# Kernel tuning notes

Measured on AMD Instinct MI355X. Metric: run time of the kernel, lower is better.

## Reference

```python
import math
import jax, jax.numpy as jnp
import numpy as np

NUM_BUCKETS = 32
MAX_DISTANCE = 128
N_HEADS = 16
D_KV = 64


def _relative_position_bucket(relative_position, num_buckets=NUM_BUCKETS, max_distance=MAX_DISTANCE):
    # bidirectional (encoder) version, faithful to T5Attention._relative_position_bucket
    nb = num_buckets // 2
    rel_buckets = (relative_position > 0).astype(jnp.int32) * nb
    rp = jnp.abs(relative_position)
    max_exact = nb // 2
    is_small = rp < max_exact
    # log-spaced buckets for large distances; clamp arg of log to >=1 to avoid -inf
    rp_large = max_exact + (
        jnp.log(jnp.maximum(rp, 1).astype(jnp.float32) / max_exact)
        / math.log(max_distance / max_exact)
        * (nb - max_exact)
    ).astype(jnp.int32)
    rp_large = jnp.minimum(rp_large, nb - 1)
    return rel_buckets + jnp.where(is_small, rp, rp_large)


def setup_inputs() -> dict:
    key = jax.random.key(0)
    ks = jax.random.split(key, 6)
    B, S, D = 2, 2048, 1024
    scale = 0.02
    return {
        "hidden_states": jax.random.normal(ks[0], (B, S, D), dtype=jnp.float32),
        "Wq": jax.random.normal(ks[1], (D, N_HEADS * D_KV), dtype=jnp.float32) * scale,
        "Wk": jax.random.normal(ks[2], (D, N_HEADS * D_KV), dtype=jnp.float32) * scale,
        "Wv": jax.random.normal(ks[3], (D, N_HEADS * D_KV), dtype=jnp.float32) * scale,
        "Wo": jax.random.normal(ks[4], (N_HEADS * D_KV, D), dtype=jnp.float32) * scale,
        "rel_bias": jax.random.normal(ks[5], (NUM_BUCKETS, N_HEADS), dtype=jnp.float32),
    }


def reference(hidden_states, Wq, Wk, Wv, Wo, rel_bias):
    B, S, D = hidden_states.shape
    H, dk = N_HEADS, D_KV
    q = (hidden_states @ Wq).reshape(B, S, H, dk)
    k = (hidden_states @ Wk).reshape(B, S, H, dk)
    v = (hidden_states @ Wv).reshape(B, S, H, dk)

    pos = jnp.arange(S)
    relative_position = pos[None, :] - pos[:, None]          # [S_q, S_k]
    buckets = _relative_position_bucket(relative_position)    # [S_q, S_k]
    bias = rel_bias[buckets].transpose(2, 0, 1)               # [H, S_q, S_k]

    # T5 attention: NO 1/sqrt(d) scaling
    scores = jnp.einsum('bqhd,bkhd->bhqk', q, k) + bias[None]
    attn = jax.nn.softmax(scores, axis=-1)
    ctx = jnp.einsum('bhqk,bkhd->bqhd', attn, v).reshape(B, S, H * dk)
    return ctx @ Wo
```

## Files before the change

kernel.cpp:

```cpp
#include <hip/hip_runtime.h>
#include <stdint.h>

#define S_LEN 2048
#define NH 16
#define NB_DELTA (2*S_LEN-1)
#define PST 72

typedef __attribute__((ext_vector_type(8))) __bf16 bf16x8;
typedef __attribute__((ext_vector_type(4))) float f32x4;

__device__ __forceinline__ unsigned short f2bf(float f){
    union { float f; unsigned int u; } v; v.f = f;
    unsigned int u = v.u;
    return (unsigned short)((u + 0x7FFFu + ((u >> 16) & 1u)) >> 16);
}
__device__ __forceinline__ unsigned short f2bf_fast(float f){
    union { float f; unsigned int u; } v; v.f = f;
    return (unsigned short)((v.u + 0x8000u) >> 16);
}
__device__ __forceinline__ float bf2f(unsigned short u){
    union { unsigned int u; float f; } v; v.u = ((unsigned int)u) << 16;
    return v.f;
}

__device__ __forceinline__ void gload16(const void* g, void* l){
    __builtin_amdgcn_global_load_lds(
        (const __attribute__((address_space(1))) void*)(uintptr_t)g,
        (__attribute__((address_space(3))) void*)(uintptr_t)l, 16, 0, 0);
}

__global__ __launch_bounds__(256) void prep_kernel(
    const float* __restrict__ hs, unsigned short* __restrict__ hsb,
    const float* __restrict__ W0, const float* __restrict__ W1,
    const float* __restrict__ W2, const float* __restrict__ W3,
    unsigned short* __restrict__ D0, unsigned short* __restrict__ D1,
    unsigned short* __restrict__ D2, unsigned short* __restrict__ D3,
    const float* __restrict__ rel_bias, float* __restrict__ biasT){
    if (blockIdx.z == 4) {
        int bi = blockIdx.y * 32 + blockIdx.x;
        for (int it = 0; it < 4; it++) {
            int i = bi * 4096 + it * 1024 + threadIdx.x * 4;
            float4 f = *(const float4*)(hs + i);
            ushort4 o;
            o.x = f2bf(f.x); o.y = f2bf(f.y); o.z = f2bf(f.z); o.w = f2bf(f.w);
            *(ushort4*)(hsb + i) = o;
        }
        if (bi < 16) {
            int t = bi * 256 + threadIdx.x;
            if (t < NB_DELTA) {
                int delta = t - (S_LEN - 1);
                int bucket = (delta > 0) ? 16 : 0;
                int a = delta < 0 ? -delta : delta;
                int b;
                if (a < 8) b = a;
                else {
                    int bl = 33 - __builtin_clz(a * a);
                    b = bl < 15 ? bl : 15;
                }
                bucket += b;
                for (int h = 0; h < NH; h++)
                    biasT[h * NB_DELTA + t] = rel_bias[bucket * NH + h];
            }
        }
        return;
    }
    const float* src; unsigned short* dst;
    switch (blockIdx.z) {
        case 0: src = W0; dst = D0; break;
        case 1: src = W1; dst = D1; break;
        case 2: src = W2; dst = D2; break;
        default: src = W3; dst = D3; break;
    }
    __shared__ float tile[32][33];
    int bx = blockIdx.x, by = blockIdx.y;
    int tx = threadIdx.x & 31, ty = threadIdx.x >> 5;
    for (int i = 0; i < 4; i++)
        tile[ty + 8*i][tx] = src[(size_t)(by*32 + ty + 8*i) * 1024 + bx*32 + tx];
    __syncthreads();
    for (int i = 0; i < 4; i++)
        dst[(size_t)(bx*32 + ty + 8*i) * 1024 + by*32 + tx] = f2bf(tile[tx][ty + 8*i]);
}

template<int MODE, int BM>
__global__ __launch_bounds__(256) void gemm_bt_kernel(const unsigned short* __restrict__ A,
                                                      const unsigned short* __restrict__ BT,
                                                      float* __restrict__ C0,
                                                      unsigned short* __restrict__ C1,
                                                      int Kdim, int ldc){
    constexpr int IT = BM / 32;
    __shared__ __align__(16) unsigned short As[BM * 64];
    __shared__ __align__(16) unsigned short Bs[128 * 64];
    const int t = threadIdx.x;
    const int wave = t >> 6, lane = t & 63;
    const int quad = lane >> 4, l16 = lane & 15;
    const int wm = (wave >> 1) * (BM / 2), wn = (wave & 1) * 64;
    const size_t row0 = (size_t)blockIdx.y * BM, col0 = (size_t)blockIdx.x * 128;

    const int srow8 = lane >> 3;
    const int gg = (lane & 7) ^ srow8;
    const unsigned short* gA = A  + (row0 + wave * 8 + srow8) * (size_t)Kdim + gg * 8;
    const unsigned short* gB = BT + (col0 + wave * 8 + srow8) * (size_t)Kdim + gg * 8;

    f32x4 acc[IT][4] = {};

    for (int kt = 0; kt < Kdim; kt += 64) {
        for (int p = 0; p < BM / 32; p++)
            gload16(gA + (size_t)(p * 32) * Kdim + kt, &As[(p * 32 + wave * 8) * 64]);
        for (int p = 0; p < 4; p++)
            gload16(gB + (size_t)(p * 32) * Kdim + kt, &Bs[(p * 32 + wave * 8) * 64]);
        __syncthreads();
        bf16x8 a[2][IT], b[2][4];
        for (int ks = 0; ks < 2; ks++) {
            for (int i = 0; i < IT; i++)
                a[ks][i] = *(const bf16x8*)(&As[(wm + i*16 + l16) * 64 + (((ks*4 + quad) ^ (l16 & 7)) * 8)]);
            for (int j = 0; j < 4; j++)
                b[ks][j] = *(const bf16x8*)(&Bs[(wn + j*16 + l16) * 64 + (((ks*4 + quad) ^ (l16 & 7)) * 8)]);
        }
        for (int ks = 0; ks < 2; ks++)
            for (int i = 0; i < IT; i++)
                for (int j = 0; j < 4; j++)
                    acc[i][j] = __builtin_amdgcn_mfma_f32_16x16x32_bf16(a[ks][i], b[ks][j], acc[i][j], 0, 0, 0);
        __syncthreads();
    }
    for (int i = 0; i < IT; i++)
        for (int j = 0; j < 4; j++) {
            size_t r0 = row0 + wm + i*16 + quad*4;
            size_t c  = col0 + wn + j*16 + l16;
            if (MODE == 0) {
                for (int r = 0; r < 4; r++)
                    C0[(r0 + r) * ldc + c] = acc[i][j][r];
            } else {
                for (int r = 0; r < 4; r++)
                    C1[(r0 + r) * ldc + c] = f2bf(acc[i][j][r]);
            }
        }
}

__global__ __launch_bounds__(256) void vtrans_kernel(const unsigned short* __restrict__ qkv,
                                                     unsigned short* __restrict__ vt){
    __shared__ unsigned short tile[64][72];
    const int v0 = blockIdx.x * 64, s0 = blockIdx.y * 64, b = blockIdx.z;
    const int tx = threadIdx.x & 7, ty = threadIdx.x >> 3;
    for (int i = 0; i < 2; i++)
        *(int4*)&tile[ty + 32*i][tx * 8] =
            *(const int4*)(qkv + (size_t)(b * 2048 + s0 + ty + 32*i) * 3072 + 2048 + v0 + tx * 8);
    __syncthreads();
    for (int i = 0; i < 2; i++) {
        int v = ty + 32*i;
        int sl = tx * 8;
        ushort4 o0, o1;
        o0.x = tile[sl+0][v]; o0.y = tile[sl+1][v]; o0.z = tile[sl+2][v]; o0.w = tile[sl+3][v];
        o1.x = tile[sl+4][v]; o1.y = tile[sl+5][v]; o1.z = tile[sl+6][v]; o1.w = tile[sl+7][v];
        unsigned short* dst = vt + (size_t)(b * 1024 + v0 + v) * 2048 + s0 + sl;
        *(ushort4*)dst = o0; *(ushort4*)(dst + 4) = o1;
    }
}

__global__ __launch_bounds__(256, 4) void flash7_kernel(
    const unsigned short* __restrict__ qkv,
    const unsigned short* __restrict__ vt,
    const float* __restrict__ biasT,
    unsigned short* __restrict__ ctxpb,
    float* __restrict__ rsbuf)
{
    const int qt = blockIdx.x, h = blockIdx.y;
    const int b = blockIdx.z >> 1, ck = blockIdx.z & 1;
    const int kt0 = ck << 10;
    const int t = threadIdx.x;
    const int w = t >> 6, lane = t & 63, quad = lane >> 4, l16 = lane & 15;
    const int q0 = qt * 128;

    __shared__ __align__(16) unsigned short Ks[64 * 64];
    __shared__ __align__(16) unsigned short Vs[64 * 64];
    __shared__ __align__(16) unsigned short Pb[128 * PST];
    __shared__ float bias_s[192];

    for (int s = 0; s < 4; s++) {
        int g = t + s * 256;
        int r = g >> 3, c = (g & 7) * 8;
        *(int4*)&Pb[r * PST + c] =
            *(const int4*)(qkv + (size_t)(b * S_LEN + q0 + r) * 3072 + h * 64 + c);
    }
    __syncthreads();
    bf16x8 qb[2][2];
    for (int nt = 0; nt < 2; nt++)
        for (int ks = 0; ks < 2; ks++)
            qb[ks][nt] = *(const bf16x8*)&Pb[(w * 32 + nt * 16 + l16) * PST + ks * 32 + quad * 8];

    float rsum[2] = {0.f, 0.f};
    f32x4 ctx[4][2] = {};

    const float* biasRow = biasT + h * NB_DELTA + 2047;

    const int srow8 = lane >> 3;
    const int gg = (lane & 7) ^ srow8;
    const int swz = ((l16 & 7) * 8);

    for (int kt = kt0; kt < kt0 + 1024; kt += 64) {
        __syncthreads();
        {
            const unsigned short* kb = qkv + (size_t)(b * S_LEN + kt + w * 8 + srow8) * 3072 + 1024 + h * 64 + gg * 8;
            const unsigned short* vb = vt + (size_t)(b * 1024 + h * 64 + w * 8 + srow8) * 2048 + kt + gg * 8;
            gload16(kb,                         &Ks[(w * 8) * 64]);
            gload16(kb + (size_t)32 * 3072,     &Ks[(32 + w * 8) * 64]);
            gload16(vb,                         &Vs[(w * 8) * 64]);
            gload16(vb + (size_t)32 * 2048,     &Vs[(32 + w * 8) * 64]);
            if (t < 192) bias_s[t] = biasRow[kt - q0 - 127 + t] - 16.0f;
        }
        __syncthreads();

        f32x4 st[4][2] = {};
        for (int ks = 0; ks < 2; ks++)
            for (int nb = 0; nb < 4; nb++) {
                bf16x8 ka = *(const bf16x8*)&Ks[(nb * 16 + l16) * 64 + (((ks * 4 + quad) * 8) ^ swz)];
                st[nb][0] = __builtin_amdgcn_mfma_f32_16x16x32_bf16(ka, qb[ks][0], st[nb][0], 0, 0, 0);
                st[nb][1] = __builtin_amdgcn_mfma_f32_16x16x32_bf16(ka, qb[ks][1], st[nb][1], 0, 0, 0);
            }
        for (int nt = 0; nt < 2; nt++) {
            const int ib = quad * 4 + 127 - w * 32 - nt * 16 - l16;
            float rs = 0.f;
            for (int nb = 0; nb < 4; nb++) {
                float e0 = __expf(st[nb][nt][0] + bias_s[ib + nb * 16 + 0]);
                float e1 = __expf(st[nb][nt][1] + bias_s[ib + nb * 16 + 1]);
                float e2 = __expf(st[nb][nt][2] + bias_s[ib + nb * 16 + 2]);
                float e3 = __expf(st[nb][nt][3] + bias_s[ib + nb * 16 + 3]);
                rs += (e0 + e1) + (e2 + e3);
                ushort4 pk;
                pk.x = f2bf_fast(e0); pk.y = f2bf_fast(e1);
                pk.z = f2bf_fast(e2); pk.w = f2bf_fast(e3);
                *(ushort4*)&Pb[(w * 32 + nt * 16 + l16) * PST + nb * 16 + quad * 4] = pk;
            }
            rsum[nt] += rs;
        }
        for (int ks = 0; ks < 2; ks++) {
            bf16x8 pb0 = *(const bf16x8*)&Pb[(w * 32 + l16) * PST + ks * 32 + quad * 8];
            bf16x8 pb1 = *(const bf16x8*)&Pb[(w * 32 + 16 + l16) * PST + ks * 32 + quad * 8];
            for (int nd = 0; nd < 4; nd++) {
                bf16x8 va = *(const bf16x8*)&Vs[(nd * 16 + l16) * 64 + (((ks * 4 + quad) * 8) ^ swz)];
                ctx[nd][0] = __builtin_amdgcn_mfma_f32_16x16x32_bf16(va, pb0, ctx[nd][0], 0, 0, 0);
                ctx[nd][1] = __builtin_amdgcn_mfma_f32_16x16x32_bf16(va, pb1, ctx[nd][1], 0, 0, 0);
            }
        }
    }
    unsigned short* cp = ctxpb + (size_t)ck * 4096 * 1024;
    for (int nt = 0; nt < 2; nt++) {
        float rs = rsum[nt];
        rs += __shfl_xor(rs, 16, 64);
        rs += __shfl_xor(rs, 32, 64);
        int row = b * S_LEN + q0 + w * 32 + nt * 16 + l16;
        if (quad == 0) rsbuf[((size_t)ck * 4096 + row) * 16 + h] = rs;
        for (int nd = 0; nd < 4; nd++) {
            ushort4 pk;
            pk.x = f2bf(ctx[nd][nt][0]); pk.y = f2bf(ctx[nd][nt][1]);
            pk.z = f2bf(ctx[nd][nt][2]); pk.w = f2bf(ctx[nd][nt][3]);
            *(ushort4*)&cp[(size_t)row * 1024 + h * 64 + nd * 16 + quad * 4] = pk;
        }
    }
}

__global__ __launch_bounds__(256) void combine_kernel(const unsigned short* __restrict__ ctxpb,
                                                      const float* __restrict__ rsbuf,
                                                      unsigned short* __restrict__ ctxb){
    int e = blockIdx.x * 256 + threadIdx.x;
    int row = e >> 8;
    int c4 = (e & 255) * 4;
    int h = c4 >> 6;
    float l = rsbuf[(size_t)row * 16 + h] + rsbuf[((size_t)4096 + row) * 16 + h];
    ushort4 a  = *(const ushort4*)&ctxpb[(size_t)row * 1024 + c4];
    ushort4 b2 = *(const ushort4*)&ctxpb[(size_t)4096 * 1024 + (size_t)row * 1024 + c4];
    float inv = 1.f / l;
    ushort4 o;
    o.x = f2bf((bf2f(a.x) + bf2f(b2.x)) * inv);
    o.y = f2bf((bf2f(a.y) + bf2f(b2.y)) * inv);
    o.z = f2bf((bf2f(a.z) + bf2f(b2.z)) * inv);
    o.w = f2bf((bf2f(a.w) + bf2f(b2.w)) * inv);
    *(ushort4*)&ctxb[(size_t)row * 1024 + c4] = o;
}

extern "C" void kernel_launch(void* const* d_in, const int* in_sizes, int n_in,
                              void* d_out, int out_size, void* d_ws, size_t ws_size,
                              hipStream_t stream) {
    const float* hs       = (const float*)d_in[0];
    const float* Wq       = (const float*)d_in[1];
    const float* Wk       = (const float*)d_in[2];
    const float* Wv       = (const float*)d_in[3];
    const float* Wo       = (const float*)d_in[4];
    const float* rel_bias = (const float*)d_in[5];
    float* out = (float*)d_out;

    char* ws = (char*)d_ws;
    float* biasT          = (float*)ws;           ws += 262144;
    unsigned short* hsb   = (unsigned short*)ws;  ws += 8388608;
    unsigned short* WT    = (unsigned short*)ws;  ws += 6291456;
    unsigned short* WoT   = (unsigned short*)ws;  ws += 2097152;
    unsigned short* qkvb  = (unsigned short*)ws;  ws += 25165824;
    unsigned short* Vtg   = (unsigned short*)ws;  ws += 8388608;
    unsigned short* ctxb  = (unsigned short*)ws;  ws += 8388608;
    unsigned short* ctxpb = (unsigned short*)ws;  ws += 16777216;
    float* rsbuf          = (float*)ws;

    prep_kernel<<<dim3(32, 32, 5), 256, 0, stream>>>(
        hs, hsb, Wq, Wk, Wv, Wo,
        WT, WT + 1024 * 1024, WT + 2 * 1024 * 1024, WoT, rel_bias, biasT);

    gemm_bt_kernel<1, 128><<<dim3(24, 32), 256, 0, stream>>>(hsb, WT, nullptr, qkvb, 1024, 3072);
    vtrans_kernel<<<dim3(16, 32, 2), 256, 0, stream>>>(qkvb, Vtg);
    flash7_kernel<<<dim3(S_LEN / 128, NH, 4), 256, 0, stream>>>(qkvb, Vtg, biasT, ctxpb, rsbuf);
    combine_kernel<<<4096, 256, 0, stream>>>(ctxpb, rsbuf, ctxb);
    gemm_bt_kernel<0, 64><<<dim3(8, 64), 256, 0, stream>>>(ctxb, WoT, out, nullptr, 1024, 1024);
}
```

Baseline: 207.6 us.

## Split flash warps over query and key halves, use exp2 with constant far-bias

Each warp in the attention kernel now covers 64 query rows and half of each 64-key tile (a 2x2 split instead of 4x1). This doubles how often each loaded K/V fragment is reused, and the two key-half partial contexts are reduced through shared memory at the end. Q is pre-scaled by log2(e) in the QKV GEMM epilogue so the softmax can use a native exp2. For key tiles far from the diagonal, the bias is the saturated bucket constant, so its load and the per-element lookup are skipped. Packed bf16 conversions replace the manual ones. The costs are higher register pressure (launch bound lowered to 3 blocks) and an extra shared-memory reduction.

```diff
diff --git a/kernel.cpp b/kernel.cpp
--- a/kernel.cpp
+++ b/kernel.cpp
@@ -1,10 +1,12 @@
 #include <hip/hip_runtime.h>
+#include <hip/hip_bf16.h>
 #include <stdint.h>
 
 #define S_LEN 2048
 #define NH 16
 #define NB_DELTA (2*S_LEN-1)
 #define PST 72
+#define LOG2E 1.4426950408889634f
 
 typedef __attribute__((ext_vector_type(8))) __bf16 bf16x8;
 typedef __attribute__((ext_vector_type(4))) float f32x4;
@@ -14,14 +16,21 @@
     unsigned int u = v.u;
     return (unsigned short)((u + 0x7FFFu + ((u >> 16) & 1u)) >> 16);
 }
-__device__ __forceinline__ unsigned short f2bf_fast(float f){
-    union { float f; unsigned int u; } v; v.f = f;
-    return (unsigned short)((v.u + 0x8000u) >> 16);
-}
 __device__ __forceinline__ float bf2f(unsigned short u){
     union { unsigned int u; float f; } v; v.u = ((unsigned int)u) << 16;
     return v.f;
 }
+__device__ __forceinline__ unsigned int pkbf(float a, float b){
+    __hip_bfloat162 h = __float22bfloat162_rn(float2{a, b});
+    unsigned int u;
+    __builtin_memcpy(&u, &h, 4);
+    return u;
+}
+#if __has_builtin(__builtin_amdgcn_exp2f)
+__device__ __forceinline__ float fexp2(float x){ return __builtin_amdgcn_exp2f(x); }
+#else
+__device__ __forceinline__ float fexp2(float x){ return __expf(x * 0.69314718056f); }
+#endif
 
 __device__ __forceinline__ void gload16(const void* g, void* l){
     __builtin_amdgcn_global_load_lds(
@@ -130,8 +139,9 @@
                 for (int r = 0; r < 4; r++)
                     C0[(r0 + r) * ldc + c] = acc[i][j][r];
             } else {
+                float qs = (c < 1024) ? LOG2E : 1.0f;
                 for (int r = 0; r < 4; r++)
-                    C1[(r0 + r) * ldc + c] = f2bf(acc[i][j][r]);
+                    C1[(r0 + r) * ldc + c] = f2bf(acc[i][j][r] * qs);
             }
         }
 }
@@ -156,10 +166,11 @@
     }
 }
 
-__global__ __launch_bounds__(256, 4) void flash7_kernel(
+__global__ __launch_bounds__(256, 3) void flash8_kernel(
     const unsigned short* __restrict__ qkv,
     const unsigned short* __restrict__ vt,
     const float* __restrict__ biasT,
+    const float* __restrict__ rel_bias,
     unsigned short* __restrict__ ctxpb,
     float* __restrict__ rsbuf)
 {
@@ -168,12 +179,17 @@
     const int kt0 = ck << 10;
     const int t = threadIdx.x;
     const int w = t >> 6, lane = t & 63, quad = lane >> 4, l16 = lane & 15;
+    const int qh = w & 1, jh = w >> 1;
     const int q0 = qt * 128;
 
-    __shared__ __align__(16) unsigned short Ks[64 * 64];
-    __shared__ __align__(16) unsigned short Vs[64 * 64];
-    __shared__ __align__(16) unsigned short Pb[128 * PST];
-    __shared__ float bias_s[192];
+    __shared__ __align__(16) unsigned short SMEM[18272];
+    unsigned short* Ks = SMEM;
+    unsigned short* Vs = SMEM + 4096;
+    unsigned short* Pb = SMEM + 8192;
+    float* bias_s = (float*)(SMEM + 17408);
+
+    const float b15 = (rel_bias[15 * NH + h] - 16.f) * LOG2E;
+    const float b31 = (rel_bias[31 * NH + h] - 16.f) * LOG2E;
 
     for (int s = 0; s < 4; s++) {
         int g = t + s * 256;
@@ -182,13 +198,13 @@
             *(const int4*)(qkv + (size_t)(b * S_LEN + q0 + r) * 3072 + h * 64 + c);
     }
     __syncthreads();
-    bf16x8 qb[2][2];
-    for (int nt = 0; nt < 2; nt++)
+    bf16x8 qb[2][4];
+    for (int nt = 0; nt < 4; nt++)
         for (int ks = 0; ks < 2; ks++)
-            qb[ks][nt] = *(const bf16x8*)&Pb[(w * 32 + nt * 16 + l16) * PST + ks * 32 + quad * 8];
-
-    float rsum[2] = {0.f, 0.f};
-    f32x4 ctx[4][2] = {};
+            qb[ks][nt] = *(const bf16x8*)&Pb[(qh * 64 + nt * 16 + l16) * PST + ks * 32 + quad * 8];
+
+    float rsum[4] = {0.f, 0.f, 0.f, 0.f};
+    f32x4 ctx[4][4] = {};
 
     const float* biasRow = biasT + h * NB_DELTA + 2047;
 
@@ -197,63 +213,94 @@
     const int swz = ((l16 & 7) * 8);
 
     for (int kt = kt0; kt < kt0 + 1024; kt += 64) {
+        const int off = kt - q0;
+        const bool cst = (off >= 255) || (off <= -191);
         __syncthreads();
         {
             const unsigned short* kb = qkv + (size_t)(b * S_LEN + kt + w * 8 + srow8) * 3072 + 1024 + h * 64 + gg * 8;
             const unsigned short* vb = vt + (size_t)(b * 1024 + h * 64 + w * 8 + srow8) * 2048 + kt + gg * 8;
-            gload16(kb,                         &Ks[(w * 8) * 64]);
-            gload16(kb + (size_t)32 * 3072,     &Ks[(32 + w * 8) * 64]);
-            gload16(vb,                         &Vs[(w * 8) * 64]);
-            gload16(vb + (size_t)32 * 2048,     &Vs[(32 + w * 8) * 64]);
-            if (t < 192) bias_s[t] = biasRow[kt - q0 - 127 + t] - 16.0f;
+            gload16(kb,                     &Ks[(w * 8) * 64]);
+            gload16(kb + (size_t)32 * 3072, &Ks[(32 + w * 8) * 64]);
+            gload16(vb,                     &Vs[(w * 8) * 64]);
+            gload16(vb + (size_t)32 * 2048, &Vs[(32 + w * 8) * 64]);
+            if (!cst && t < 192) bias_s[t] = (biasRow[off - 127 + t] - 16.f) * LOG2E;
         }
         __syncthreads();
 
-        f32x4 st[4][2] = {};
+        f32x4 st[2][4] = {};
         for (int ks = 0; ks < 2; ks++)
-            for (int nb = 0; nb < 4; nb++) {
-                bf16x8 ka = *(const bf16x8*)&Ks[(nb * 16 + l16) * 64 + (((ks * 4 + quad) * 8) ^ swz)];
-                st[nb][0] = __builtin_amdgcn_mfma_f32_16x16x32_bf16(ka, qb[ks][0], st[nb][0], 0, 0, 0);
-                st[nb][1] = __builtin_amdgcn_mfma_f32_16x16x32_bf16(ka, qb[ks][1], st[nb][1], 0, 0, 0);
-            }
-        for (int nt = 0; nt < 2; nt++) {
-            const int ib = quad * 4 + 127 - w * 32 - nt * 16 - l16;
+            for (int nb = 0; nb < 2; nb++) {
+                bf16x8 ka = *(const bf16x8*)&Ks[(jh * 32 + nb * 16 + l16) * 64 + (((ks * 4 + quad) * 8) ^ swz)];
+                for (int nt = 0; nt < 4; nt++)
+                    st[nb][nt] = __builtin_amdgcn_mfma_f32_16x16x32_bf16(ka, qb[ks][nt], st[nb][nt], 0, 0, 0);
+            }
+        const float bc = (off > 0) ? b31 : b15;
+        for (int nt = 0; nt < 4; nt++) {
+            const int ib = jh * 32 + quad * 4 + 127 - qh * 64 - nt * 16 - l16;
             float rs = 0.f;
-            for (int nb = 0; nb < 4; nb++) {
-                float e0 = __expf(st[nb][nt][0] + bias_s[ib + nb * 16 + 0]);
-                float e1 = __expf(st[nb][nt][1] + bias_s[ib + nb * 16 + 1]);
-                float e2 = __expf(st[nb][nt][2] + bias_s[ib + nb * 16 + 2]);
-                float e3 = __expf(st[nb][nt][3] + bias_s[ib + nb * 16 + 3]);
+            for (int nb = 0; nb < 2; nb++) {
+                float e0, e1, e2, e3;
+                if (cst) {
+                    e0 = fexp2(st[nb][nt][0] + bc);
+                    e1 = fexp2(st[nb][nt][1] + bc);
+                    e2 = fexp2(st[nb][nt][2] + bc);
+                    e3 = fexp2(st[nb][nt][3] + bc);
+                } else {
+                    e0 = fexp2(st[nb][nt][0] + bias_s[ib + nb * 16 + 0]);
+                    e1 = fexp2(st[nb][nt][1] + bias_s[ib + nb * 16 + 1]);
+                    e2 = fexp2(st[nb][nt][2] + bias_s[ib + nb * 16 + 2]);
+                    e3 = fexp2(st[nb][nt][3] + bias_s[ib + nb * 16 + 3]);
+                }
                 rs += (e0 + e1) + (e2 + e3);
-                ushort4 pk;
-                pk.x = f2bf_fast(e0); pk.y = f2bf_fast(e1);
-                pk.z = f2bf_fast(e2); pk.w = f2bf_fast(e3);
-                *(ushort4*)&Pb[(w * 32 + nt * 16 + l16) * PST + nb * 16 + quad * 4] = pk;
+                uint2 pk; pk.x = pkbf(e0, e1); pk.y = pkbf(e2, e3);
+                *(uint2*)&Pb[(qh * 64 + nt * 16 + l16) * PST + jh * 32 + nb * 16 + quad * 4] = pk;
             }
             rsum[nt] += rs;
         }
-        for (int ks = 0; ks < 2; ks++) {
-            bf16x8 pb0 = *(const bf16x8*)&Pb[(w * 32 + l16) * PST + ks * 32 + quad * 8];
-            bf16x8 pb1 = *(const bf16x8*)&Pb[(w * 32 + 16 + l16) * PST + ks * 32 + quad * 8];
-            for (int nd = 0; nd < 4; nd++) {
-                bf16x8 va = *(const bf16x8*)&Vs[(nd * 16 + l16) * 64 + (((ks * 4 + quad) * 8) ^ swz)];
-                ctx[nd][0] = __builtin_amdgcn_mfma_f32_16x16x32_bf16(va, pb0, ctx[nd][0], 0, 0, 0);
-                ctx[nd][1] = __builtin_amdgcn_mfma_f32_16x16x32_bf16(va, pb1, ctx[nd][1], 0, 0, 0);
-            }
-        }
-    }
-    unsigned short* cp = ctxpb + (size_t)ck * 4096 * 1024;
-    for (int nt = 0; nt < 2; nt++) {
+        bf16x8 pb[4];
+        for (int nt = 0; nt < 4; nt++)
+            pb[nt] = *(const bf16x8*)&Pb[(qh * 64 + nt * 16 + l16) * PST + jh * 32 + quad * 8];
+        for (int nd = 0; nd < 4; nd++) {
+            bf16x8 va = *(const bf16x8*)&Vs[(nd * 16 + l16) * 64 + (((jh * 4 + quad) * 8) ^ swz)];
+            for (int nt = 0; nt < 4; nt++)
+                ctx[nd][nt] = __builtin_amdgcn_mfma_f32_16x16x32_bf16(va, pb[nt], ctx[nd][nt], 0, 0, 0);
+        }
+    }
+    __syncthreads();
+    float* fscr = (float*)SMEM;
+    float rsq[4];
+    for (int nt = 0; nt < 4; nt++) {
         float rs = rsum[nt];
         rs += __shfl_xor(rs, 16, 64);
         rs += __shfl_xor(rs, 32, 64);
-        int row = b * S_LEN + q0 + w * 32 + nt * 16 + l16;
-        if (quad == 0) rsbuf[((size_t)ck * 4096 + row) * 16 + h] = rs;
-        for (int nd = 0; nd < 4; nd++) {
-            ushort4 pk;
-            pk.x = f2bf(ctx[nd][nt][0]); pk.y = f2bf(ctx[nd][nt][1]);
-            pk.z = f2bf(ctx[nd][nt][2]); pk.w = f2bf(ctx[nd][nt][3]);
-            *(ushort4*)&cp[(size_t)row * 1024 + h * 64 + nd * 16 + quad * 4] = pk;
+        rsq[nt] = rs;
+    }
+    if (jh == 1) {
+        float* dst = fscr + (qh << 12) + lane * 4;
+        for (int nd = 0; nd < 4; nd++)
+            for (int nt = 0; nt < 4; nt++)
+                *(f32x4*)(dst + (nd * 4 + nt) * 256) = ctx[nd][nt];
+        if (quad == 0)
+            for (int nt = 0; nt < 4; nt++)
+                fscr[8192 + (qh << 6) + nt * 16 + l16] = rsq[nt];
+    }
+    __syncthreads();
+    if (jh == 0) {
+        float* src = fscr + (qh << 12) + lane * 4;
+        for (int nd = 0; nd < 4; nd++)
+            for (int nt = 0; nt < 4; nt++)
+                ctx[nd][nt] += *(const f32x4*)(src + (nd * 4 + nt) * 256);
+        unsigned short* cp = ctxpb + (size_t)ck * 4096 * 1024;
+        for (int nt = 0; nt < 4; nt++) {
+            float rst = rsq[nt] + fscr[8192 + (qh << 6) + nt * 16 + l16];
+            int row = b * S_LEN + q0 + qh * 64 + nt * 16 + l16;
+            if (quad == 0) rsbuf[((size_t)ck * 4096 + row) * 16 + h] = rst;
+            for (int nd = 0; nd < 4; nd++) {
+                uint2 pk;
+                pk.x = pkbf(ctx[nd][nt][0], ctx[nd][nt][1]);
+                pk.y = pkbf(ctx[nd][nt][2], ctx[nd][nt][3]);
+                *(uint2*)&cp[(size_t)row * 1024 + h * 64 + nd * 16 + quad * 4] = pk;
+            }
         }
     }
 }
@@ -269,12 +316,10 @@
     ushort4 a  = *(const ushort4*)&ctxpb[(size_t)row * 1024 + c4];
     ushort4 b2 = *(const ushort4*)&ctxpb[(size_t)4096 * 1024 + (size_t)row * 1024 + c4];
     float inv = 1.f / l;
-    ushort4 o;
-    o.x = f2bf((bf2f(a.x) + bf2f(b2.x)) * inv);
-    o.y = f2bf((bf2f(a.y) + bf2f(b2.y)) * inv);
-    o.z = f2bf((bf2f(a.z) + bf2f(b2.z)) * inv);
-    o.w = f2bf((bf2f(a.w) + bf2f(b2.w)) * inv);
-    *(ushort4*)&ctxb[(size_t)row * 1024 + c4] = o;
+    uint2 o;
+    o.x = pkbf((bf2f(a.x) + bf2f(b2.x)) * inv, (bf2f(a.y) + bf2f(b2.y)) * inv);
+    o.y = pkbf((bf2f(a.z) + bf2f(b2.z)) * inv, (bf2f(a.w) + bf2f(b2.w)) * inv);
+    *(uint2*)&ctxb[(size_t)row * 1024 + c4] = o;
 }
 
 extern "C" void kernel_launch(void* const* d_in, const int* in_sizes, int n_in,
@@ -305,7 +350,7 @@
 
     gemm_bt_kernel<1, 128><<<dim3(24, 32), 256, 0, stream>>>(hsb, WT, nullptr, qkvb, 1024, 3072);
     vtrans_kernel<<<dim3(16, 32, 2), 256, 0, stream>>>(qkvb, Vtg);
-    flash7_kernel<<<dim3(S_LEN / 128, NH, 4), 256, 0, stream>>>(qkvb, Vtg, biasT, ctxpb, rsbuf);
+    flash8_kernel<<<dim3(S_LEN / 128, NH, 4), 256, 0, stream>>>(qkvb, Vtg, biasT, rel_bias, ctxpb, rsbuf);
     combine_kernel<<<4096, 256, 0, stream>>>(ctxpb, rsbuf, ctxb);
     gemm_bt_kernel<0, 64><<<dim3(8, 64), 256, 0, stream>>>(ctxb, WoT, out, nullptr, 1024, 1024);
 }
```

Result: slower. 223.6 us (+7.7%).
